# Kernel tuning notes

Measured on AMD Instinct MI355X. Metric: run time of the kernel, lower is better.

Reference implementation:

```python
import jax, jax.numpy as jnp
import numpy as np

N = 8192
E = 131072
NODE_DIM = 128
HIDDEN_DIM = 256


def setup_inputs() -> dict:
    key = jax.random.key(0)
    k1, k2, k3 = jax.random.split(key, 3)
    x = jax.random.normal(k1, (N, NODE_DIM), dtype=jnp.float32)
    edge_index = jax.random.randint(k2, (2, E), 0, N, dtype=jnp.int64)
    # nn.Linear(node_dim, hidden_dim, bias=False): weight [hidden_dim, node_dim]
    W = jax.random.normal(k3, (HIDDEN_DIM, NODE_DIM), dtype=jnp.float32) * (1.0 / np.sqrt(NODE_DIM))
    return {"x": x, "edge_index": edge_index, "W": W}


def reference(x, edge_index, W):
    num_nodes = x.shape[0]
    src, tgt = edge_index[0], edge_index[1]
    # Dense adjacency: A[src, tgt] = 1 (set semantics, duplicates collapse)
    A = jnp.zeros((num_nodes, num_nodes), dtype=x.dtype).at[src, tgt].set(1.0)
    A_tilde = A + jnp.eye(num_nodes, dtype=x.dtype)
    D = A_tilde.sum(axis=1)
    D_inv_sqrt = D ** -0.5
    # D_tilde @ A_tilde @ D_tilde == row/col scaling of A_tilde
    A_hat = D_inv_sqrt[:, None] * A_tilde * D_inv_sqrt[None, :]
    out = A_hat @ x            # [N, node_dim]
    out = out @ W.T            # [N, hidden_dim]
    return out
```

## Files before the change

### kernel.cpp

```cpp
#include <hip/hip_runtime.h>

#define N_NODES 8192
#define NODE_DIM 128
#define HIDDEN_DIM 256
#define WORDS_PER_ROW 256
#define CAP 96
#define RPB 16
#define YLD 136

typedef __attribute__((ext_vector_type(8))) short bf16x8;
typedef __attribute__((ext_vector_type(4))) float f32x4;

static __device__ __forceinline__ unsigned short f2bf(float f) {
    unsigned u = __builtin_bit_cast(unsigned, f);
    unsigned r = u + 0x7fffu + ((u >> 16) & 1u);
    return (unsigned short)(r >> 16);
}
static __device__ __forceinline__ float bf2f(unsigned short h) {
    unsigned u = ((unsigned)h) << 16;
    return __builtin_bit_cast(float, u);
}

__global__ void dedupe_kernel(const int* __restrict__ e,
                              unsigned int* __restrict__ bitmask,
                              unsigned int* __restrict__ deg,
                              int* __restrict__ rowlist,
                              const float* __restrict__ W,
                              unsigned short* __restrict__ wh,
                              unsigned short* __restrict__ wl,
                              int E, int nEdgeBlocks) {
    if ((int)blockIdx.x < nEdgeBlocks) {
        int idx = blockIdx.x * 256 + threadIdx.x;
        if (idx >= E) return;
        int s = e[idx];
        int t = e[E + idx];
        unsigned int w = (unsigned int)s * WORDS_PER_ROW + ((unsigned int)t >> 5);
        unsigned int m = 1u << (t & 31);
        unsigned int old = atomicOr(&bitmask[w], m);
        if (!(old & m)) {
            unsigned int p = atomicAdd(&deg[s], 1u);
            if (p < CAP) rowlist[(size_t)s * CAP + p] = t;
        }
    } else {
        int t = (blockIdx.x - nEdgeBlocks) * 256 + threadIdx.x;
        if (t >= HIDDEN_DIM * NODE_DIM / 4) return;
        float4 v = ((const float4*)W)[t];
        ushort4 h, l;
        h.x = f2bf(v.x); l.x = f2bf(v.x - bf2f(h.x));
        h.y = f2bf(v.y); l.y = f2bf(v.y - bf2f(h.y));
        h.z = f2bf(v.z); l.z = f2bf(v.z - bf2f(h.z));
        h.w = f2bf(v.w); l.w = f2bf(v.w - bf2f(h.w));
        ((ushort4*)wh)[t] = h;
        ((ushort4*)wl)[t] = l;
    }
}

__global__ __launch_bounds__(512)
void fused_agg_gemm(const int* __restrict__ rowlist,
                    const unsigned int* __restrict__ deg,
                    const float* __restrict__ x,
                    const unsigned short* __restrict__ Wh,
                    const unsigned short* __restrict__ Wl,
                    float* __restrict__ out) {
    __shared__ int            nrow[RPB];
    __shared__ float          sdi[RPB];
    __shared__ int            cols[RPB][CAP];
    __shared__ float          djs[RPB][CAP];
    __shared__ unsigned short Yh[RPB][YLD];
    __shared__ unsigned short Yl[RPB][YLD];

    int tid = threadIdx.x;
    int m0  = blockIdx.x * RPB;

    if (tid < RPB) {
        unsigned int dg = deg[m0 + tid];
        int n = (int)dg; if (n > CAP) n = CAP;
        nrow[tid] = n;
        sdi[tid]  = rsqrtf((float)dg + 1.0f);
    }
    __syncthreads();

    for (int e = tid; e < RPB * CAP; e += 512) {
        int r = e / CAP, k = e - r * CAP;
        if (k < nrow[r]) {
            int c = rowlist[(size_t)(m0 + r) * CAP + k];
            cols[r][k] = c;
            djs[r][k]  = rsqrtf((float)deg[c] + 1.0f);
        }
    }
    __syncthreads();

    {
        int team = tid >> 5;
        int l4   = tid & 31;
        const float4* x4 = (const float4*)x;
        int   n    = nrow[team];
        float di   = sdi[team];
        float4 self = x4[(size_t)(m0 + team) * 32 + l4];
        float ax = 0.f, ay = 0.f, az = 0.f, aw = 0.f;
        int k = 0;
        for (; k + 2 <= n; k += 2) {
            float  d0 = djs[team][k];
            float  d1 = djs[team][k + 1];
            float4 v0 = x4[(size_t)cols[team][k]     * 32 + l4];
            float4 v1 = x4[(size_t)cols[team][k + 1] * 32 + l4];
            ax += d0 * v0.x + d1 * v1.x;
            ay += d0 * v0.y + d1 * v1.y;
            az += d0 * v0.z + d1 * v1.z;
            aw += d0 * v0.w + d1 * v1.w;
        }
        if (k < n) {
            float  d0 = djs[team][k];
            float4 v0 = x4[(size_t)cols[team][k] * 32 + l4];
            ax += d0 * v0.x; ay += d0 * v0.y; az += d0 * v0.z; aw += d0 * v0.w;
        }
        float vx = di * (di * self.x + ax);
        float vy = di * (di * self.y + ay);
        float vz = di * (di * self.z + az);
        float vw = di * (di * self.w + aw);
        ushort4 h, l;
        h.x = f2bf(vx); l.x = f2bf(vx - bf2f(h.x));
        h.y = f2bf(vy); l.y = f2bf(vy - bf2f(h.y));
        h.z = f2bf(vz); l.z = f2bf(vz - bf2f(h.z));
        h.w = f2bf(vw); l.w = f2bf(vw - bf2f(h.w));
        *(ushort4*)&Yh[team][l4 * 4] = h;
        *(ushort4*)&Yl[team][l4 * 4] = l;
    }
    __syncthreads();

    {
        int wave = tid >> 6;
        int lane = tid & 63;
        int quad = lane >> 4;
        int l16  = lane & 15;

        f32x4 acc[2] = {{0,0,0,0},{0,0,0,0}};
#pragma unroll
        for (int ks = 0; ks < 4; ++ks) {
            bf16x8 ah = *(const bf16x8*)&Yh[l16][ks * 32 + quad * 8];
            bf16x8 al = *(const bf16x8*)&Yl[l16][ks * 32 + quad * 8];
#pragma unroll
            for (int ct = 0; ct < 2; ++ct) {
                int hcol = wave * 32 + ct * 16 + l16;
                bf16x8 bh = *(const bf16x8*)(Wh + (size_t)hcol * NODE_DIM + ks * 32 + quad * 8);
                bf16x8 bl = *(const bf16x8*)(Wl + (size_t)hcol * NODE_DIM + ks * 32 + quad * 8);
                acc[ct] = __builtin_amdgcn_mfma_f32_16x16x32_bf16(ah, bh, acc[ct], 0, 0, 0);
                acc[ct] = __builtin_amdgcn_mfma_f32_16x16x32_bf16(ah, bl, acc[ct], 0, 0, 0);
                acc[ct] = __builtin_amdgcn_mfma_f32_16x16x32_bf16(al, bh, acc[ct], 0, 0, 0);
            }
        }
#pragma unroll
        for (int ct = 0; ct < 2; ++ct) {
#pragma unroll
            for (int r = 0; r < 4; ++r) {
                out[(size_t)(m0 + quad * 4 + r) * HIDDEN_DIM + wave * 32 + ct * 16 + l16] = acc[ct][r];
            }
        }
    }
}

extern "C" void kernel_launch(void* const* d_in, const int* in_sizes, int n_in,
                              void* d_out, int out_size, void* d_ws, size_t ws_size,
                              hipStream_t stream) {
    const float* x = (const float*)d_in[0];
    const int*   e = (const int*)d_in[1];
    const float* W = (const float*)d_in[2];
    float*       out = (float*)d_out;
    int E = in_sizes[1] / 2;

    unsigned int*   bitmask = (unsigned int*)d_ws;
    unsigned int*   deg     = bitmask + (size_t)N_NODES * WORDS_PER_ROW;
    int*            rowlist = (int*)(deg + N_NODES);
    unsigned short* wh      = (unsigned short*)(rowlist + (size_t)N_NODES * CAP);
    unsigned short* wl      = wh + (size_t)HIDDEN_DIM * NODE_DIM;

    size_t clear_bytes = ((size_t)N_NODES * WORDS_PER_ROW + N_NODES) * sizeof(unsigned int);
    hipMemsetAsync(d_ws, 0, clear_bytes, stream);

    int nEdgeBlocks = (E + 255) / 256;
    int nWBlocks    = (HIDDEN_DIM * NODE_DIM / 4 + 255) / 256;
    dedupe_kernel<<<nEdgeBlocks + nWBlocks, 256, 0, stream>>>(e, bitmask, deg, rowlist,
                                                              W, wh, wl, E, nEdgeBlocks);
    fused_agg_gemm<<<N_NODES / RPB, 512, 0, stream>>>(rowlist, deg, x, wh, wl, out);
}
```

Baseline: 91.21 us.

## Replace bitmask edge dedupe with append-then-compact per-row deduplication

Drops the dense N×N bitmask and its 8 MB memset, along with the per-edge atomicOr. Every edge is now appended to its source row's list unconditionally. A new compact kernel then removes duplicate targets within each row, one wavefront per row, using a quadratic scan plus a ballot/popcount compaction, and rewrites the degree. The costs are an extra kernel launch and a cap of 64 raw edges per row, so rows with more raw edges are silently truncated.

New measurement: 90.27 us, median of 2. About the same (-1.0%).

```diff
diff --git a/kernel.cpp b/kernel.cpp
--- a/kernel.cpp
+++ b/kernel.cpp
@@ -3,7 +3,6 @@
 #define N_NODES 8192
 #define NODE_DIM 128
 #define HIDDEN_DIM 256
-#define WORDS_PER_ROW 256
 #define CAP 96
 #define RPB 16
 #define YLD 136
@@ -21,8 +20,7 @@
     return __builtin_bit_cast(float, u);
 }
 
-__global__ void dedupe_kernel(const int* __restrict__ e,
-                              unsigned int* __restrict__ bitmask,
+__global__ void append_kernel(const int* __restrict__ e,
                               unsigned int* __restrict__ deg,
                               int* __restrict__ rowlist,
                               const float* __restrict__ W,
@@ -34,13 +32,8 @@
         if (idx >= E) return;
         int s = e[idx];
         int t = e[E + idx];
-        unsigned int w = (unsigned int)s * WORDS_PER_ROW + ((unsigned int)t >> 5);
-        unsigned int m = 1u << (t & 31);
-        unsigned int old = atomicOr(&bitmask[w], m);
-        if (!(old & m)) {
-            unsigned int p = atomicAdd(&deg[s], 1u);
-            if (p < CAP) rowlist[(size_t)s * CAP + p] = t;
-        }
+        unsigned int p = atomicAdd(&deg[s], 1u);
+        if (p < CAP) rowlist[(size_t)s * CAP + p] = t;
     } else {
         int t = (blockIdx.x - nEdgeBlocks) * 256 + threadIdx.x;
         if (t >= HIDDEN_DIM * NODE_DIM / 4) return;
@@ -53,6 +46,31 @@
         ((ushort4*)wh)[t] = h;
         ((ushort4*)wl)[t] = l;
     }
+}
+
+__global__ __launch_bounds__(256)
+void compact_kernel(int* __restrict__ rowlist, unsigned int* __restrict__ deg) {
+    __shared__ int buf[4][64];
+    int w    = threadIdx.x >> 6;
+    int lane = threadIdx.x & 63;
+    int i    = blockIdx.x * 4 + w;
+    int n = (int)deg[i];
+    if (n > 64) n = 64;
+    int t = -1;
+    if (lane < n) t = rowlist[(size_t)i * CAP + lane];
+    buf[w][lane] = t;
+    __syncthreads();
+    bool keep = false;
+    if (lane < n) {
+        keep = true;
+        for (int j = 0; j < lane; ++j) {
+            if (buf[w][j] == t) { keep = false; break; }
+        }
+    }
+    unsigned long long m = __ballot(keep);
+    int pos = __popcll(m & ((1ull << lane) - 1ull));
+    if (keep && pos != lane) rowlist[(size_t)i * CAP + pos] = t;
+    if (lane == 0) deg[i] = (unsigned int)__popcll(m);
 }
 
 __global__ __launch_bounds__(512)
@@ -168,18 +186,17 @@
     float*       out = (float*)d_out;
     int E = in_sizes[1] / 2;
 
-    unsigned int*   bitmask = (unsigned int*)d_ws;
-    unsigned int*   deg     = bitmask + (size_t)N_NODES * WORDS_PER_ROW;
+    unsigned int*   deg     = (unsigned int*)d_ws;
     int*            rowlist = (int*)(deg + N_NODES);
     unsigned short* wh      = (unsigned short*)(rowlist + (size_t)N_NODES * CAP);
     unsigned short* wl      = wh + (size_t)HIDDEN_DIM * NODE_DIM;
 
-    size_t clear_bytes = ((size_t)N_NODES * WORDS_PER_ROW + N_NODES) * sizeof(unsigned int);
-    hipMemsetAsync(d_ws, 0, clear_bytes, stream);
+    hipMemsetAsync(d_ws, 0, (size_t)N_NODES * sizeof(unsigned int), stream);
 
     int nEdgeBlocks = (E + 255) / 256;
     int nWBlocks    = (HIDDEN_DIM * NODE_DIM / 4 + 255) / 256;
-    dedupe_kernel<<<nEdgeBlocks + nWBlocks, 256, 0, stream>>>(e, bitmask, deg, rowlist,
+    append_kernel<<<nEdgeBlocks + nWBlocks, 256, 0, stream>>>(e, deg, rowlist,
                                                               W, wh, wl, E, nEdgeBlocks);
+    compact_kernel<<<N_NODES / 4, 256, 0, stream>>>(rowlist, deg);
     fused_agg_gemm<<<N_NODES / RPB, 512, 0, stream>>>(rowlist, deg, x, wh, wl, out);
 }
```
